# Optimization experiments

Hardware: AMD Instinct MI355X
Metric: run time of the kernel (lower is better)

## Reference

```python
import jax, jax.numpy as jnp
import numpy as np
from jax import lax

N_NODES = 100000
L_IN = 60           # raw per-node signal length
DEG = 16            # in-degree per node
HID = 256           # hidden_dim = 64 * (L_IN/15)
HEADS = 2
OUT = HID // 2      # GATConv out_feats per head
EPS_BN = 1e-5
COS_S = 4.6


def setup_inputs() -> dict:
    key = jax.random.key(0)
    k = jax.random.split(key, 12)
    E = N_NODES * DEG
    x = jax.random.normal(k[0], (N_NODES, L_IN), jnp.float32)
    src = jax.random.randint(k[1], (E,), 0, N_NODES, jnp.int32)
    # every node receives DEG incoming edges (DGL GATConv requires nonzero in-degree)
    dst = jnp.repeat(jnp.arange(N_NODES, dtype=jnp.int32), DEG)
    n = lambda i, s, sc=0.05: jax.random.normal(k[i], s, jnp.float32) * sc
    return dict(
        x=x, src=src, dst=dst,
        w1=n(2, (32, 1, 5), 0.2), b1=jnp.zeros(32, jnp.float32),
        bn1_g=jnp.ones(32, jnp.float32), bn1_b=jnp.zeros(32, jnp.float32),
        w2=n(3, (64, 32, 3), 0.1), b2=jnp.zeros(64, jnp.float32),
        bn2_g=jnp.ones(64, jnp.float32), bn2_b=jnp.zeros(64, jnp.float32),
        fc1_w=n(4, (HEADS * OUT, HID)), attn1_l=n(5, (HEADS, OUT)), attn1_r=n(6, (HEADS, OUT)),
        bias1=jnp.zeros(HEADS * OUT, jnp.float32),
        fc2_w=n(7, (HEADS * OUT, HID)), attn2_l=n(8, (HEADS, OUT)), attn2_r=n(9, (HEADS, OUT)),
        bias2=jnp.zeros(HEADS * OUT, jnp.float32),
        dbn_g=jnp.ones(3 * HID, jnp.float32), dbn_b=jnp.zeros(3 * HID, jnp.float32),
        cos_W=n(10, (HID, 3 * HID), 1.0),
    )


def _conv_bn_relu(h, w, b, g, bt, stride):
    # h: [N, Cin, T] -> [N, Cout, T'] ; BatchNorm1d uses batch statistics (train-mode forward)
    y = lax.conv_general_dilated(h, w, (stride,), 'VALID',
                                 dimension_numbers=('NCH', 'OIH', 'NCH'))
    y = y + b[None, :, None]
    m = jnp.mean(y, (0, 2), keepdims=True)
    v = jnp.var(y, (0, 2), keepdims=True)
    y = (y - m) / jnp.sqrt(v + EPS_BN) * g[None, :, None] + bt[None, :, None]
    return jax.nn.relu(y)


def _gat(h, fc_w, al, ar, bias, src, dst):
    # DGL GATConv: fc -> edge attention (leaky_relu 0.2) -> edge softmax over dst -> weighted sum + bias
    feat = (h @ fc_w.T).reshape(N_NODES, HEADS, OUT)          # [N,H,D]
    el = jnp.sum(feat * al[None], -1)                          # [N,H]
    er = jnp.sum(feat * ar[None], -1)                          # [N,H]
    e = jax.nn.leaky_relu(el[src] + er[dst], 0.2)              # [E,H]
    emax = jax.ops.segment_max(e, dst, num_segments=N_NODES)  # [N,H]
    emax = jnp.where(jnp.isfinite(emax), emax, 0.0)
    ex = jnp.exp(e - emax[dst])
    den = jax.ops.segment_sum(ex, dst, num_segments=N_NODES)  # [N,H]
    alpha = ex / jnp.maximum(den[dst], 1e-12)                  # [E,H]
    out = jax.ops.segment_sum(feat[src] * alpha[..., None], dst, num_segments=N_NODES)
    return out + bias.reshape(1, HEADS, OUT)                   # [N,H,D]


def _l2n(a):
    # F.normalize: divide by L2 norm clamped to eps
    return a / jnp.maximum(jnp.linalg.norm(a, axis=1, keepdims=True), 1e-12)


def reference(x, src, dst, w1, b1, bn1_g, bn1_b, w2, b2, bn2_g, bn2_b,
              fc1_w, attn1_l, attn1_r, bias1, fc2_w, attn2_l, attn2_r, bias2,
              dbn_g, dbn_b, cos_W):
    h = x[:, None, :]                                    # [N,1,L]
    h = _conv_bn_relu(h, w1, b1, bn1_g, bn1_b, 5)        # [N,32,12]
    h = _conv_bn_relu(h, w2, b2, bn2_g, bn2_b, 3)        # [N,64,4]
    h = h.reshape(N_NODES, HID)                          # [N,256]
    g1 = _gat(h, fc1_w, attn1_l, attn1_r, bias1, src, dst)
    h1 = (jax.nn.relu(g1) + jnp.tanh(g1) + jax.nn.log_sigmoid(g1)).reshape(N_NODES, HID)
    h2 = jnp.tanh(_gat(h1, fc2_w, attn2_l, attn2_r, bias2, src, dst)).reshape(N_NODES, HID)
    h3 = jax.nn.relu(_gat(h2, fc2_w, attn2_l, attn2_r, bias2, src, dst)).reshape(N_NODES, HID)
    hc = jnp.concatenate([h1, h2, h3], axis=1)           # [N,768]
    m = jnp.mean(hc, 0)
    v = jnp.var(hc, 0)
    hc = (hc - m) / jnp.sqrt(v + EPS_BN) * dbn_g + dbn_b
    return _l2n(hc) @ _l2n(cos_W).T * COS_S              # [N,256]
```

## Files before the change

### kernel.cpp

```cpp
#include <hip/hip_runtime.h>

#define NN 100000
#define MPAD 100096
#define NT_M 782

typedef unsigned short u16;
typedef _Float16 f16x8 __attribute__((ext_vector_type(8)));
typedef __attribute__((ext_vector_type(4))) float f32x4;

__device__ __forceinline__ u16 f2h(float f){
  union { _Float16 h; u16 u; } v; v.h=(_Float16)f; return v.u;
}
__device__ __forceinline__ float h2f(u16 u){
  union { u16 u; _Float16 h; } v; v.u=u; return (float)v.h;
}
__device__ __forceinline__ void gload16(const void* g, void* l){
  __builtin_amdgcn_global_load_lds((const __attribute__((address_space(1))) void*)g,
                                   (__attribute__((address_space(3))) void*)l, 16, 0, 0);
}
__device__ __forceinline__ void lds_fence(){
  asm volatile("s_waitcnt lgkmcnt(0)" ::: "memory");
  __builtin_amdgcn_wave_barrier();
}

template<int EPI>
__global__ __launch_bounds__(256) void k_gemm(
  const u16* __restrict__ a0, const u16* __restrict__ a1, const u16* __restrict__ a2,
  const u16* __restrict__ bmat, u16* __restrict__ cout,
  float* __restrict__ outf, const float* __restrict__ tvec,
  const float* __restrict__ rnorm, int Bstride, int KT)
{
  __shared__ u16 lds[2][2][8192];
  const int tid=threadIdx.x, lane=tid&63, wid=tid>>6;
  const int wr=wid>>1, wc=wid&1;
  const long m0=(long)blockIdx.x*128;
  const int n0=blockIdx.y*128;
  f32x4 acc[4][4]={};

  auto stageT=[&](u16* L, const u16* G, long rs){
    #pragma unroll
    for(int i=0;i<4;i++){
      int idx=i*256+tid;
      int row=idx>>3, slot=idx&7;
      int gc=(slot^(row&7))*8;
      gload16(G+(long)row*rs+gc, L+idx*8);
    }
  };
  auto stage=[&](int buf,int kt){
    const u16* Ab=(kt<4)?a0:((kt<8)?a1:a2);
    int kc=(kt&3)*64;
    stageT(lds[buf][0], Ab+m0*256+kc, 256);
    stageT(lds[buf][1], bmat+(long)n0*Bstride+kt*64, Bstride);
  };
  stage(0,0);
  __syncthreads();
  int buf=0;
  for(int kt=0;kt<KT;kt++){
    if(kt+1<KT) stage(buf^1,kt+1);
    const u16* LA=lds[buf][0]; const u16* LB=lds[buf][1];
    #pragma unroll
    for(int kk=0;kk<2;kk++){
      f16x8 av[4], bv[4];
      #pragma unroll
      for(int mf=0;mf<4;mf++){
        int r=wr*64+mf*16+(lane&15);
        av[mf]=*(const f16x8*)&LA[r*64 + (((kk*4+(lane>>4))^(r&7))*8)];
      }
      #pragma unroll
      for(int nf=0;nf<4;nf++){
        int r=wc*64+nf*16+(lane&15);
        bv[nf]=*(const f16x8*)&LB[r*64 + (((kk*4+(lane>>4))^(r&7))*8)];
      }
      #pragma unroll
      for(int mf=0;mf<4;mf++){
        #pragma unroll
        for(int nf=0;nf<4;nf++)
          acc[mf][nf]=__builtin_amdgcn_mfma_f32_16x16x32_f16(av[mf],bv[nf],acc[mf][nf],0,0,0);
      }
    }
    __syncthreads();
    buf^=1;
  }
  #pragma unroll
  for(int mf=0;mf<4;mf++){
    #pragma unroll
    for(int j=0;j<4;j++){
      long row=m0+wr*64+mf*16+((lane>>4)*4)+j;
      if(row<NN){
        #pragma unroll
        for(int nf=0;nf<4;nf++){
          int col=n0+wc*64+nf*16+(lane&15);
          float v=acc[mf][nf][j];
          if(EPI==1) outf[row*256+col]=(v+tvec[col])*rnorm[row];
          else       cout[row*256+col]=f2h(v);
        }
      }
    }
  }
}

__global__ __launch_bounds__(256) void k_xmom(const float* __restrict__ x, float* __restrict__ stats){
  int t=blockIdx.x*blockDim.x+threadIdx.x, stride=gridDim.x*blockDim.x;
  int lane=threadIdx.x&63;
  float m[5]={0,0,0,0,0};
  float c[15]={0,0,0,0,0,0,0,0,0,0,0,0,0,0,0};
  for(int n=t;n<NN;n+=stride){
    float xr[60];
    #pragma unroll
    for(int i=0;i<15;i++){
      float4 v=*(const float4*)&x[(long)n*60+i*4];
      xr[i*4]=v.x; xr[i*4+1]=v.y; xr[i*4+2]=v.z; xr[i*4+3]=v.w;
    }
    #pragma unroll
    for(int p=0;p<12;p++){
      float vv[5]={xr[5*p],xr[5*p+1],xr[5*p+2],xr[5*p+3],xr[5*p+4]};
      #pragma unroll
      for(int k=0;k<5;k++) m[k]+=vv[k];
      int idx=0;
      #pragma unroll
      for(int k=0;k<5;k++){
        #pragma unroll
        for(int k2=k;k2<5;k2++){ c[idx]+=vv[k]*vv[k2]; idx++; }
      }
    }
  }
  float vals[20];
  #pragma unroll
  for(int i=0;i<5;i++) vals[i]=m[i];
  #pragma unroll
  for(int i=0;i<15;i++) vals[5+i]=c[i];
  #pragma unroll
  for(int i=0;i<20;i++){
    float v=vals[i];
    #pragma unroll
    for(int off=32;off;off>>=1) v+=__shfl_xor(v,off);
    if(lane==0) atomicAdd(&stats[i],v);
  }
}

__global__ void k_fin1(const float* __restrict__ stats, const float* __restrict__ w1,
                       const float* __restrict__ b1, const float* __restrict__ g,
                       const float* __restrict__ bt, float* __restrict__ a1c1){
  int c=threadIdx.x;
  if(c>=32) return;
  const float inv=1.0f/(NN*12.0f);
  float mu[5];
  for(int k=0;k<5;k++) mu[k]=stats[k]*inv;
  float C[5][5];
  int idx=5;
  for(int k=0;k<5;k++) for(int k2=k;k2<5;k2++){ float v=stats[idx++]*inv; C[k][k2]=v; C[k2][k]=v; }
  float wv[5];
  for(int k=0;k<5;k++) wv[k]=w1[c*5+k];
  float bb=b1[c];
  float mean=bb, e2=bb*bb;
  for(int k=0;k<5;k++){ mean+=wv[k]*mu[k]; e2+=2.f*bb*wv[k]*mu[k]; }
  for(int k=0;k<5;k++) for(int k2=0;k2<5;k2++) e2+=wv[k]*wv[k2]*C[k][k2];
  float var=e2-mean*mean;
  float a=g[c]*rsqrtf(var+1e-5f);
  a1c1[c]=a; a1c1[32+c]=bt[c]-mean*a;
}

__global__ void k_prep(const float* __restrict__ fc1, const float* __restrict__ fc2,
                       const float* __restrict__ a1l, const float* __restrict__ a1r,
                       const float* __restrict__ a2l, const float* __restrict__ a2r,
                       float* __restrict__ vprep){
  int k=threadIdx.x;
  float acc[8]={0,0,0,0,0,0,0,0};
  for(int r=0;r<256;r++){
    int h=r>>7, c=r&127;
    float f1=fc1[r*256+k], f2=fc2[r*256+k];
    acc[0+h]+=f1*a1l[h*128+c];
    acc[2+h]+=f1*a1r[h*128+c];
    acc[4+h]+=f2*a2l[h*128+c];
    acc[6+h]+=f2*a2r[h*128+c];
  }
  #pragma unroll
  for(int v=0;v<8;v++) vprep[v*256+k]=acc[v];
}

__global__ __launch_bounds__(256) void k_conv(const float* __restrict__ x,
  const float* __restrict__ w1, const float* __restrict__ b1,
  const float* __restrict__ a1c1, const float* __restrict__ w2,
  const float* __restrict__ b2, float* __restrict__ y2, float* __restrict__ stats2)
{
  __shared__ float w2s[64*97];
  __shared__ float w1s[160], a1s[32], c1s[32], b1s[32], b2s[64];
  __shared__ float xs[4][64];
  __shared__ float z1s[4][384];
  __shared__ float bsum[128];
  int tid=threadIdx.x, lane=tid&63, w=tid>>6;
  for(int i=tid;i<6144;i+=256) w2s[(i/96)*97+(i%96)]=w2[i];
  if(tid<160) w1s[tid]=w1[tid];
  if(tid<32){ a1s[tid]=a1c1[tid]; c1s[tid]=a1c1[32+tid]; b1s[tid]=b1[tid]; }
  if(tid<64) b2s[tid]=b2[tid];
  if(tid<128) bsum[tid]=0.f;
  __syncthreads();
  float ssum=0.f, ssq=0.f;
  int gw=blockIdx.x*4+w, nw=gridDim.x*4;
  for(int n=gw;n<NN;n+=nw){
    if(lane<60) xs[w][lane]=x[(long)n*60+lane];
    lds_fence();
    {
      int c=lane>>1, pb=(lane&1)*6;
      float av=a1s[c], cv=c1s[c], bb=b1s[c];
      #pragma unroll
      for(int i=0;i<6;i++){
        int p=pb+i;
        float y=bb;
        #pragma unroll
        for(int k=0;k<5;k++) y+=xs[w][5*p+k]*w1s[c*5+k];
        z1s[w][c*12+p]=fmaxf(y*av+cv,0.f);
      }
    }
    lds_fence();
    {
      int c2=lane;
      float acc0=b2s[c2],acc1=b2s[c2],acc2=b2s[c2],acc3=b2s[c2];
      #pragma unroll
      for(int ci=0;ci<32;ci++){
        float4 za=*(const float4*)&z1s[w][ci*12];
        float4 zb=*(const float4*)&z1s[w][ci*12+4];
        float4 zc=*(const float4*)&z1s[w][ci*12+8];
        float w0=w2s[c2*97+ci*3], wv1=w2s[c2*97+ci*3+1], wv2=w2s[c2*97+ci*3+2];
        acc0 += za.x*w0+za.y*wv1+za.z*wv2;
        acc1 += za.w*w0+zb.x*wv1+zb.y*wv2;
        acc2 += zb.z*w0+zb.w*wv1+zc.x*wv2;
        acc3 += zc.y*w0+zc.z*wv1+zc.w*wv2;
      }
      float4 o; o.x=acc0; o.y=acc1; o.z=acc2; o.w=acc3;
      *(float4*)&y2[(long)n*256+c2*4]=o;
      ssum+=acc0+acc1+acc2+acc3;
      ssq+=acc0*acc0+acc1*acc1+acc2*acc2+acc3*acc3;
    }
    lds_fence();
  }
  atomicAdd(&bsum[lane],ssum);
  atomicAdd(&bsum[64+lane],ssq);
  __syncthreads();
  if(tid<128) atomicAdd(&stats2[tid],bsum[tid]);
}

__global__ void k_fin2(const float* __restrict__ stats2, const float* __restrict__ g,
                       const float* __restrict__ bt, float* __restrict__ a2c2){
  int c=threadIdx.x;
  if(c>=64) return;
  const float inv=1.0f/(NN*4.0f);
  float mean=stats2[c]*inv;
  float var=stats2[64+c]*inv-mean*mean;
  float a=g[c]*rsqrtf(var+1e-5f);
  a2c2[c]=a; a2c2[64+c]=bt[c]-mean*a;
}

__global__ __launch_bounds__(256) void k_happ(const float* __restrict__ y2,
  const float* __restrict__ a2c2, const float* __restrict__ vprep,
  u16* __restrict__ h, float* __restrict__ elv, float* __restrict__ erv)
{
  int lane=threadIdx.x&63;
  int gw=blockIdx.x*4+(threadIdx.x>>6), nw=gridDim.x*4;
  float a2=a2c2[lane], c2v=a2c2[64+lane];
  int cb=lane*4;
  float4 vl0=*(const float4*)&vprep[cb];
  float4 vl1=*(const float4*)&vprep[256+cb];
  float4 vr0=*(const float4*)&vprep[512+cb];
  float4 vr1=*(const float4*)&vprep[768+cb];
  for(int n=gw;n<NN;n+=nw){
    float4 y=*(const float4*)&y2[(long)n*256+cb];
    float o0=fmaxf(y.x*a2+c2v,0.f), o1=fmaxf(y.y*a2+c2v,0.f);
    float o2=fmaxf(y.z*a2+c2v,0.f), o3=fmaxf(y.w*a2+c2v,0.f);
    ushort4 o; o.x=f2h(o0); o.y=f2h(o1); o.z=f2h(o2); o.w=f2h(o3);
    *(ushort4*)&h[(long)n*256+cb]=o;
    float pl0=o0*vl0.x+o1*vl0.y+o2*vl0.z+o3*vl0.w;
    float pl1=o0*vl1.x+o1*vl1.y+o2*vl1.z+o3*vl1.w;
    float pr0=o0*vr0.x+o1*vr0.y+o2*vr0.z+o3*vr0.w;
    float pr1=o0*vr1.x+o1*vr1.y+o2*vr1.z+o3*vr1.w;
    #pragma unroll
    for(int off=32;off;off>>=1){
      pl0+=__shfl_xor(pl0,off); pl1+=__shfl_xor(pl1,off);
      pr0+=__shfl_xor(pr0,off); pr1+=__shfl_xor(pr1,off);
    }
    if(lane==0){ elv[2*n]=pl0; elv[2*n+1]=pl1; erv[2*n]=pr0; erv[2*n+1]=pr1; }
  }
}

__global__ void k_cvth(const float* __restrict__ in, u16* __restrict__ out, int n){
  int i=blockIdx.x*blockDim.x+threadIdx.x;
  if(i<n) out[i]=f2h(in[i]);
}

__global__ __launch_bounds__(256) void k_wfold(const float* __restrict__ cw, const float* __restrict__ ab,
  u16* __restrict__ wh, float* __restrict__ tvec)
{
  int lane=threadIdx.x&63;
  int r=blockIdx.x*4+(threadIdx.x>>6);
  if(r>=256) return;
  float v[12]; float ss=0.f, tn=0.f;
  #pragma unroll
  for(int i=0;i<12;i++){
    int col=i*64+lane;
    v[i]=cw[r*768+col];
    ss+=v[i]*v[i];
    tn+=v[i]*ab[768+col];
  }
  #pragma unroll
  for(int off=32;off;off>>=1){ ss+=__shfl_xor(ss,off); tn+=__shfl_xor(tn,off); }
  float sc=1.0f/fmaxf(sqrtf(ss),1e-12f);
  #pragma unroll
  for(int i=0;i<12;i++){
    int col=i*64+lane;
    wh[r*768+col]=f2h(v[i]*sc*ab[col]);
  }
  if(lane==0) tvec[r]=tn*sc;
}

__global__ __launch_bounds__(256) void k_alpha(const float* __restrict__ el, const float* __restrict__ er,
  const int* __restrict__ srcv, float* __restrict__ alpha)
{
  int n=blockIdx.x*blockDim.x+threadIdx.x;
  if(n>=NN) return;
  int sidx[16];
  #pragma unroll
  for(int j=0;j<16;j+=4){
    int4 v=*(const int4*)&srcv[n*16+j];
    sidx[j]=v.x; sidx[j+1]=v.y; sidx[j+2]=v.z; sidx[j+3]=v.w;
  }
  float er0=er[2*n], er1=er[2*n+1];
  float e0[16], e1[16];
  float mx0=-1e30f, mx1=-1e30f;
  #pragma unroll
  for(int j=0;j<16;j++){
    float a=el[2*sidx[j]]+er0;
    float bb=el[2*sidx[j]+1]+er1;
    a = a>0.f? a : 0.2f*a;
    bb = bb>0.f? bb : 0.2f*bb;
    e0[j]=a; e1[j]=bb;
    mx0=fmaxf(mx0,a); mx1=fmaxf(mx1,bb);
  }
  float d0=0.f,d1=0.f;
  #pragma unroll
  for(int j=0;j<16;j++){
    e0[j]=__expf(e0[j]-mx0); d0+=e0[j];
    e1[j]=__expf(e1[j]-mx1); d1+=e1[j];
  }
  float r0=1.f/fmaxf(d0,1e-12f), r1=1.f/fmaxf(d1,1e-12f);
  #pragma unroll
  for(int j=0;j<16;j++){
    float2 o; o.x=e0[j]*r0; o.y=e1[j]*r1;
    ((float2*)alpha)[(long)n*16+j]=o;
  }
}

template<int ACT> __device__ __forceinline__ float actf(float g);
template<> __device__ __forceinline__ float actf<1>(float g){
  float t=tanhf(g);
  float ls=fminf(g,0.f)-log1pf(__expf(-fabsf(g)));
  return fmaxf(g,0.f)+t+ls;
}
template<> __device__ __forceinline__ float actf<2>(float g){ return tanhf(g); }
template<> __device__ __forceinline__ float actf<3>(float g){ return fmaxf(g,0.f); }

template<int ACT,int WELR>
__global__ __launch_bounds__(256) void k_aggr(const u16* __restrict__ fH,
  const float* __restrict__ alpha, const int* __restrict__ srcv, const float* __restrict__ bias,
  u16* __restrict__ hH, float* __restrict__ dbn_raw, int col_base,
  const float* __restrict__ vnext, float* __restrict__ elo, float* __restrict__ ero)
{
  __shared__ float bsum[256], bsq[256];
  int tid=threadIdx.x, lane=tid&63;
  bsum[tid]=0.f; bsq[tid]=0.f;
  __syncthreads();
  int gw=blockIdx.x*4+(tid>>6), nw=gridDim.x*4;
  int head=lane>>5, cb=lane*4;
  float4 b4=*(const float4*)&bias[cb];
  float4 vl0={0,0,0,0},vl1={0,0,0,0},vr0={0,0,0,0},vr1={0,0,0,0};
  if(WELR){
    vl0=*(const float4*)&vnext[cb];
    vl1=*(const float4*)&vnext[256+cb];
    vr0=*(const float4*)&vnext[512+cb];
    vr1=*(const float4*)&vnext[768+cb];
  }
  float s[4]={0,0,0,0}, q[4]={0,0,0,0};
  for(int n=gw;n<NN;n+=nw){
    int sidx[16];
    #pragma unroll
    for(int j=0;j<16;j+=4){
      int4 v=*(const int4*)&srcv[n*16+j];
      sidx[j]=v.x; sidx[j+1]=v.y; sidx[j+2]=v.z; sidx[j+3]=v.w;
    }
    float a0=b4.x,a1=b4.y,a2=b4.z,a3=b4.w;
    #pragma unroll
    for(int j=0;j<16;j++){
      float2 aw2=((const float2*)alpha)[(long)n*16+j];
      float aw = head? aw2.y : aw2.x;
      ushort4 f=*(const ushort4*)&fH[(long)sidx[j]*256+cb];
      a0+=aw*h2f(f.x); a1+=aw*h2f(f.y);
      a2+=aw*h2f(f.z); a3+=aw*h2f(f.w);
    }
    float h0=actf<ACT>(a0), h1=actf<ACT>(a1), h2=actf<ACT>(a2), h3=actf<ACT>(a3);
    ushort4 o; o.x=f2h(h0); o.y=f2h(h1); o.z=f2h(h2); o.w=f2h(h3);
    *(ushort4*)&hH[(long)n*256+cb]=o;
    s[0]+=h0; s[1]+=h1; s[2]+=h2; s[3]+=h3;
    q[0]+=h0*h0; q[1]+=h1*h1; q[2]+=h2*h2; q[3]+=h3*h3;
    if(WELR){
      float pl0=h0*vl0.x+h1*vl0.y+h2*vl0.z+h3*vl0.w;
      float pl1=h0*vl1.x+h1*vl1.y+h2*vl1.z+h3*vl1.w;
      float pr0=h0*vr0.x+h1*vr0.y+h2*vr0.z+h3*vr0.w;
      float pr1=h0*vr1.x+h1*vr1.y+h2*vr1.z+h3*vr1.w;
      #pragma unroll
      for(int off2=32;off2;off2>>=1){
        pl0+=__shfl_xor(pl0,off2); pl1+=__shfl_xor(pl1,off2);
        pr0+=__shfl_xor(pr0,off2); pr1+=__shfl_xor(pr1,off2);
      }
      if(lane==0){ elo[2*n]=pl0; elo[2*n+1]=pl1; ero[2*n]=pr0; ero[2*n+1]=pr1; }
    }
  }
  #pragma unroll
  for(int i=0;i<4;i++){ atomicAdd(&bsum[cb+i], s[i]); atomicAdd(&bsq[cb+i], q[i]); }
  __syncthreads();
  atomicAdd(&dbn_raw[col_base+tid], bsum[tid]);
  atomicAdd(&dbn_raw[768+col_base+tid], bsq[tid]);
}

__global__ void k_dbnfin(const float* __restrict__ raw, const float* __restrict__ g,
                         const float* __restrict__ b, float* __restrict__ ab){
  int c=blockIdx.x*blockDim.x+threadIdx.x;
  if(c<768){
    float mean=raw[c]*(1.0f/NN);
    float var=raw[768+c]*(1.0f/NN)-mean*mean;
    float a=g[c]*rsqrtf(var+1e-5f);
    ab[c]=a; ab[768+c]=b[c]-mean*a;
  }
}

__global__ __launch_bounds__(256) void k_rnorm(
  const u16* __restrict__ h1h, const u16* __restrict__ h2h, const u16* __restrict__ h3h,
  const float* __restrict__ ab, float* __restrict__ rn)
{
  int lane=threadIdx.x&63;
  int gw=blockIdx.x*4+(threadIdx.x>>6), nw=gridDim.x*4;
  int cb=lane*4;
  float av[12], cv[12];
  #pragma unroll
  for(int s=0;s<3;s++){
    #pragma unroll
    for(int i=0;i<4;i++){ av[s*4+i]=ab[s*256+cb+i]; cv[s*4+i]=ab[768+s*256+cb+i]; }
  }
  for(int n=gw;n<NN;n+=nw){
    float ss=0.f;
    const u16* hh[3]={h1h,h2h,h3h};
    #pragma unroll
    for(int s=0;s<3;s++){
      ushort4 a4=*(const ushort4*)&hh[s][(long)n*256+cb];
      float o0=h2f(a4.x)*av[s*4+0]+cv[s*4+0];
      float o1=h2f(a4.y)*av[s*4+1]+cv[s*4+1];
      float o2=h2f(a4.z)*av[s*4+2]+cv[s*4+2];
      float o3=h2f(a4.w)*av[s*4+3]+cv[s*4+3];
      ss+=o0*o0+o1*o1+o2*o2+o3*o3;
    }
    #pragma unroll
    for(int off=32;off;off>>=1) ss+=__shfl_xor(ss,off);
    if(lane==0) rn[n]=4.6f/fmaxf(sqrtf(ss),1e-12f);
  }
}

extern "C" void kernel_launch(void* const* d_in, const int* in_sizes, int n_in,
                              void* d_out, int out_size, void* d_ws, size_t ws_size,
                              hipStream_t stream)
{
  (void)in_sizes; (void)n_in; (void)out_size; (void)ws_size;
  const float* x   =(const float*)d_in[0];
  const int*   src =(const int*)d_in[1];
  const float* w1  =(const float*)d_in[3];
  const float* b1  =(const float*)d_in[4];
  const float* bn1g=(const float*)d_in[5];
  const float* bn1b=(const float*)d_in[6];
  const float* w2  =(const float*)d_in[7];
  const float* b2  =(const float*)d_in[8];
  const float* bn2g=(const float*)d_in[9];
  const float* bn2b=(const float*)d_in[10];
  const float* fc1 =(const float*)d_in[11];
  const float* a1l =(const float*)d_in[12];
  const float* a1r =(const float*)d_in[13];
  const float* bias1=(const float*)d_in[14];
  const float* fc2 =(const float*)d_in[15];
  const float* a2l =(const float*)d_in[16];
  const float* a2r =(const float*)d_in[17];
  const float* bias2=(const float*)d_in[18];
  const float* dbng=(const float*)d_in[19];
  const float* dbnb=(const float*)d_in[20];
  const float* cw  =(const float*)d_in[21];

  char* ws=(char*)d_ws;
  size_t off=0;
  auto take=[&](size_t bytes)->char*{ char* p=ws+off; off=(off+bytes+255)&~(size_t)255; return p; };
  float* stats =(float*)take(2048*4);
  float* params=(float*)take(4096*4);
  float* el    =(float*)take((size_t)MPAD*2*4);
  float* er    =(float*)take((size_t)MPAD*2*4);
  float* rnorm =(float*)take((size_t)MPAD*4);
  float* tvec  =(float*)take(256*4);
  float* alpha =(float*)take((size_t)NN*32*4);
  u16* fc1h=(u16*)take((size_t)65536*2);
  u16* fc2h=(u16*)take((size_t)65536*2);
  u16* wfh =(u16*)take((size_t)196608*2);
  float* y2 =(float*)take((size_t)MPAD*256*4);
  const size_t FB=(size_t)MPAD*256*2;
  u16* h0H  =(u16*)take(FB);
  u16* h1H  =(u16*)take(FB);
  u16* h2H  =(u16*)take(FB);
  u16* featH=(u16*)d_out;

  float* xmom   =stats;
  float* stats2 =stats+32;
  float* dbn_raw=stats+512;
  float* a1c1   =params;
  float* a2c2   =params+64;
  float* dbn_ab =params+256;
  float* vprep  =params+2048;

  hipMemsetAsync(stats,0,2048*4,stream);
  k_cvth<<<dim3(256),dim3(256),0,stream>>>(fc1,fc1h,65536);
  k_cvth<<<dim3(256),dim3(256),0,stream>>>(fc2,fc2h,65536);
  k_prep<<<dim3(1),dim3(256),0,stream>>>(fc1,fc2,a1l,a1r,a2l,a2r,vprep);
  k_xmom<<<dim3(128),dim3(256),0,stream>>>(x,xmom);
  k_fin1<<<dim3(1),dim3(64),0,stream>>>(xmom,w1,b1,bn1g,bn1b,a1c1);
  k_conv<<<dim3(1024),dim3(256),0,stream>>>(x,w1,b1,a1c1,w2,b2,y2,stats2);
  k_fin2<<<dim3(1),dim3(64),0,stream>>>(stats2,bn2g,bn2b,a2c2);
  k_happ<<<dim3(2048),dim3(256),0,stream>>>(y2,a2c2,vprep,h0H,el,er);

  dim3 gg(NT_M,2);
  k_gemm<0><<<gg,dim3(256),0,stream>>>(h0H,h0H,h0H,fc1h,featH,(float*)nullptr,tvec,rnorm,256,4);
  k_alpha<<<dim3(391),dim3(256),0,stream>>>(el,er,src,alpha);
  k_aggr<1,1><<<dim3(2048),dim3(256),0,stream>>>(featH,alpha,src,bias1,h1H,dbn_raw,0,
                                                 vprep+1024,el,er);
  k_gemm<0><<<gg,dim3(256),0,stream>>>(h1H,h1H,h1H,fc2h,featH,(float*)nullptr,tvec,rnorm,256,4);
  k_alpha<<<dim3(391),dim3(256),0,stream>>>(el,er,src,alpha);
  k_aggr<2,1><<<dim3(2048),dim3(256),0,stream>>>(featH,alpha,src,bias2,h2H,dbn_raw,256,
                                                 vprep+1024,el,er);
  k_gemm<0><<<gg,dim3(256),0,stream>>>(h2H,h2H,h2H,fc2h,featH,(float*)nullptr,tvec,rnorm,256,4);
  k_alpha<<<dim3(391),dim3(256),0,stream>>>(el,er,src,alpha);
  k_aggr<3,0><<<dim3(2048),dim3(256),0,stream>>>(featH,alpha,src,bias2,h0H,dbn_raw,512,
                                                 vprep+1024,el,er);
  k_dbnfin<<<dim3(3),dim3(256),0,stream>>>(dbn_raw,dbng,dbnb,dbn_ab);
  k_wfold<<<dim3(64),dim3(256),0,stream>>>(cw,dbn_ab,wfh,tvec);
  k_rnorm<<<dim3(1024),dim3(256),0,stream>>>(h1H,h2H,h0H,dbn_ab,rnorm);
  k_gemm<1><<<gg,dim3(256),0,stream>>>(h1H,h2H,h0H,wfh,(u16*)nullptr,
                                       (float*)d_out,tvec,rnorm,768,12);
}
```

Measured before the change: 1.259 ms.

## Recast second conv layer as fp16 MFMA GEMM with fused column statistics

```diff
diff --git a/kernel.cpp b/kernel.cpp
--- a/kernel.cpp
+++ b/kernel.cpp
@@ -28,14 +28,17 @@
   const u16* __restrict__ a0, const u16* __restrict__ a1, const u16* __restrict__ a2,
   const u16* __restrict__ bmat, u16* __restrict__ cout,
   float* __restrict__ outf, const float* __restrict__ tvec,
-  const float* __restrict__ rnorm, int Bstride, int KT)
+  const float* __restrict__ rnorm, float* __restrict__ colstats,
+  int CW, int Bstride, int KT)
 {
   __shared__ u16 lds[2][2][8192];
+  __shared__ float cstat[256];
   const int tid=threadIdx.x, lane=tid&63, wid=tid>>6;
   const int wr=wid>>1, wc=wid&1;
   const long m0=(long)blockIdx.x*128;
   const int n0=blockIdx.y*128;
   f32x4 acc[4][4]={};
+  if(EPI==2) cstat[tid]=0.f;
 
   auto stageT=[&](u16* L, const u16* G, long rs){
     #pragma unroll
@@ -47,10 +50,12 @@
     }
   };
   auto stage=[&](int buf,int kt){
-    const u16* Ab=(kt<4)?a0:((kt<8)?a1:a2);
-    int kc=(kt&3)*64;
-    stageT(lds[buf][0], Ab+m0*256+kc, 256);
-    stageT(lds[buf][1], bmat+(long)n0*Bstride+kt*64, Bstride);
+    int kg=kt*64;
+    int chn=kg/CW;
+    int kc=kg-chn*CW;
+    const u16* Ab = (chn==0)?a0:((chn==1)?a1:a2);
+    stageT(lds[buf][0], Ab+m0*CW+kc, CW);
+    stageT(lds[buf][1], bmat+(long)n0*Bstride+kg, Bstride);
   };
   stage(0,0);
   __syncthreads();
@@ -81,6 +86,7 @@
     __syncthreads();
     buf^=1;
   }
+  float csum[4]={0,0,0,0}, csq[4]={0,0,0,0};
   #pragma unroll
   for(int mf=0;mf<4;mf++){
     #pragma unroll
@@ -92,9 +98,23 @@
           int col=n0+wc*64+nf*16+(lane&15);
           float v=acc[mf][nf][j];
           if(EPI==1) outf[row*256+col]=(v+tvec[col])*rnorm[row];
-          else       cout[row*256+col]=f2h(v);
+          else if(EPI==2){ outf[row*256+col]=v; csum[nf]+=v; csq[nf]+=v*v; }
+          else cout[row*256+col]=f2h(v);
         }
       }
+    }
+  }
+  if(EPI==2){
+    #pragma unroll
+    for(int nf=0;nf<4;nf++){
+      int lc=wc*64+nf*16+(lane&15);
+      atomicAdd(&cstat[lc],csum[nf]);
+      atomicAdd(&cstat[128+lc],csq[nf]);
+    }
+    __syncthreads();
+    if(tid<128){
+      atomicAdd(&colstats[n0+tid],cstat[tid]);
+      atomicAdd(&colstats[256+n0+tid],cstat[128+tid]);
     }
   }
 }
@@ -178,75 +198,62 @@
   for(int v=0;v<8;v++) vprep[v*256+k]=acc[v];
 }
 
-__global__ __launch_bounds__(256) void k_conv(const float* __restrict__ x,
+__global__ void k_w2d(const float* __restrict__ w2, u16* __restrict__ wd){
+  int j=threadIdx.x;
+  if(j>=256) return;
+  int c2=j>>2, p=j&3;
+  for(int t=0;t<384;t++) wd[j*384+t]=0;
+  for(int ci=0;ci<32;ci++)
+    for(int k=0;k<3;k++)
+      wd[j*384 + ci*12 + 3*p + k]=f2h(w2[(c2*32+ci)*3+k]);
+}
+
+__global__ __launch_bounds__(256) void k_z1(const float* __restrict__ x,
   const float* __restrict__ w1, const float* __restrict__ b1,
-  const float* __restrict__ a1c1, const float* __restrict__ w2,
-  const float* __restrict__ b2, float* __restrict__ y2, float* __restrict__ stats2)
-{
-  __shared__ float w2s[64*97];
-  __shared__ float w1s[160], a1s[32], c1s[32], b1s[32], b2s[64];
+  const float* __restrict__ a1c1, u16* __restrict__ z1)
+{
+  __shared__ float w1s[160], a1s[32], c1s[32], b1s[32];
   __shared__ float xs[4][64];
-  __shared__ float z1s[4][384];
-  __shared__ float bsum[128];
   int tid=threadIdx.x, lane=tid&63, w=tid>>6;
-  for(int i=tid;i<6144;i+=256) w2s[(i/96)*97+(i%96)]=w2[i];
   if(tid<160) w1s[tid]=w1[tid];
   if(tid<32){ a1s[tid]=a1c1[tid]; c1s[tid]=a1c1[32+tid]; b1s[tid]=b1[tid]; }
-  if(tid<64) b2s[tid]=b2[tid];
-  if(tid<128) bsum[tid]=0.f;
   __syncthreads();
-  float ssum=0.f, ssq=0.f;
   int gw=blockIdx.x*4+w, nw=gridDim.x*4;
+  int c=lane>>1, pb=(lane&1)*6;
+  float av=a1s[c], cv=c1s[c], bb=b1s[c];
+  float wv[5];
+  #pragma unroll
+  for(int k=0;k<5;k++) wv[k]=w1s[c*5+k];
   for(int n=gw;n<NN;n+=nw){
     if(lane<60) xs[w][lane]=x[(long)n*60+lane];
     lds_fence();
-    {
-      int c=lane>>1, pb=(lane&1)*6;
-      float av=a1s[c], cv=c1s[c], bb=b1s[c];
-      #pragma unroll
-      for(int i=0;i<6;i++){
-        int p=pb+i;
-        float y=bb;
-        #pragma unroll
-        for(int k=0;k<5;k++) y+=xs[w][5*p+k]*w1s[c*5+k];
-        z1s[w][c*12+p]=fmaxf(y*av+cv,0.f);
-      }
-    }
+    ushort2 zz[3];
+    #pragma unroll
+    for(int i=0;i<6;i++){
+      int p=pb+i;
+      float y=bb;
+      #pragma unroll
+      for(int k=0;k<5;k++) y+=xs[w][5*p+k]*wv[k];
+      u16 h=f2h(fmaxf(y*av+cv,0.f));
+      if(i&1) zz[i>>1].y=h; else zz[i>>1].x=h;
+    }
+    long base=(long)n*384 + c*12 + pb;
+    *(ushort2*)&z1[base]  =zz[0];
+    *(ushort2*)&z1[base+2]=zz[1];
+    *(ushort2*)&z1[base+4]=zz[2];
     lds_fence();
-    {
-      int c2=lane;
-      float acc0=b2s[c2],acc1=b2s[c2],acc2=b2s[c2],acc3=b2s[c2];
-      #pragma unroll
-      for(int ci=0;ci<32;ci++){
-        float4 za=*(const float4*)&z1s[w][ci*12];
-        float4 zb=*(const float4*)&z1s[w][ci*12+4];
-        float4 zc=*(const float4*)&z1s[w][ci*12+8];
-        float w0=w2s[c2*97+ci*3], wv1=w2s[c2*97+ci*3+1], wv2=w2s[c2*97+ci*3+2];
-        acc0 += za.x*w0+za.y*wv1+za.z*wv2;
-        acc1 += za.w*w0+zb.x*wv1+zb.y*wv2;
-        acc2 += zb.z*w0+zb.w*wv1+zc.x*wv2;
-        acc3 += zc.y*w0+zc.z*wv1+zc.w*wv2;
-      }
-      float4 o; o.x=acc0; o.y=acc1; o.z=acc2; o.w=acc3;
-      *(float4*)&y2[(long)n*256+c2*4]=o;
-      ssum+=acc0+acc1+acc2+acc3;
-      ssq+=acc0*acc0+acc1*acc1+acc2*acc2+acc3*acc3;
-    }
-    lds_fence();
-  }
-  atomicAdd(&bsum[lane],ssum);
-  atomicAdd(&bsum[64+lane],ssq);
-  __syncthreads();
-  if(tid<128) atomicAdd(&stats2[tid],bsum[tid]);
-}
-
-__global__ void k_fin2(const float* __restrict__ stats2, const float* __restrict__ g,
+  }
+}
+
+__global__ void k_fin2(const float* __restrict__ cs, const float* __restrict__ g,
                        const float* __restrict__ bt, float* __restrict__ a2c2){
   int c=threadIdx.x;
   if(c>=64) return;
+  float s=cs[4*c]+cs[4*c+1]+cs[4*c+2]+cs[4*c+3];
+  float q=cs[256+4*c]+cs[256+4*c+1]+cs[256+4*c+2]+cs[256+4*c+3];
   const float inv=1.0f/(NN*4.0f);
-  float mean=stats2[c]*inv;
-  float var=stats2[64+c]*inv-mean*mean;
+  float mean=s*inv;
+  float var=q*inv-mean*mean;
   float a=g[c]*rsqrtf(var+1e-5f);
   a2c2[c]=a; a2c2[64+c]=bt[c]-mean*a;
 }
@@ -492,7 +499,7 @@
   char* ws=(char*)d_ws;
   size_t off=0;
   auto take=[&](size_t bytes)->char*{ char* p=ws+off; off=(off+bytes+255)&~(size_t)255; return p; };
-  float* stats =(float*)take(2048*4);
+  float* stats =(float*)take(4096*4);
   float* params=(float*)take(4096*4);
   float* el    =(float*)take((size_t)MPAD*2*4);
   float* er    =(float*)take((size_t)MPAD*2*4);
@@ -502,6 +509,8 @@
   u16* fc1h=(u16*)take((size_t)65536*2);
   u16* fc2h=(u16*)take((size_t)65536*2);
   u16* wfh =(u16*)take((size_t)196608*2);
+  u16* w2d =(u16*)take((size_t)98304*2);
+  u16* z1  =(u16*)take((size_t)MPAD*384*2);
   float* y2 =(float*)take((size_t)MPAD*256*4);
   const size_t FB=(size_t)MPAD*256*2;
   u16* h0H  =(u16*)take(FB);
@@ -510,33 +519,40 @@
   u16* featH=(u16*)d_out;
 
   float* xmom   =stats;
-  float* stats2 =stats+32;
-  float* dbn_raw=stats+512;
+  float* stats2 =stats+64;
+  float* dbn_raw=stats+1024;
   float* a1c1   =params;
   float* a2c2   =params+64;
   float* dbn_ab =params+256;
   float* vprep  =params+2048;
 
-  hipMemsetAsync(stats,0,2048*4,stream);
+  hipMemsetAsync(stats,0,4096*4,stream);
   k_cvth<<<dim3(256),dim3(256),0,stream>>>(fc1,fc1h,65536);
   k_cvth<<<dim3(256),dim3(256),0,stream>>>(fc2,fc2h,65536);
   k_prep<<<dim3(1),dim3(256),0,stream>>>(fc1,fc2,a1l,a1r,a2l,a2r,vprep);
+  k_w2d<<<dim3(1),dim3(256),0,stream>>>(w2,w2d);
   k_xmom<<<dim3(128),dim3(256),0,stream>>>(x,xmom);
   k_fin1<<<dim3(1),dim3(64),0,stream>>>(xmom,w1,b1,bn1g,bn1b,a1c1);
-  k_conv<<<dim3(1024),dim3(256),0,stream>>>(x,w1,b1,a1c1,w2,b2,y2,stats2);
+  k_z1<<<dim3(1024),dim3(256),0,stream>>>(x,w1,b1,a1c1,z1);
+
+  dim3 gg(NT_M,2);
+  k_gemm<2><<<gg,dim3(256),0,stream>>>(z1,z1,z1,w2d,(u16*)nullptr,y2,
+                                       (float*)nullptr,(float*)nullptr,stats2,384,384,6);
   k_fin2<<<dim3(1),dim3(64),0,stream>>>(stats2,bn2g,bn2b,a2c2);
   k_happ<<<dim3(2048),dim3(256),0,stream>>>(y2,a2c2,vprep,h0H,el,er);
 
-  dim3 gg(NT_M,2);
-  k_gemm<0><<<gg,dim3(256),0,stream>>>(h0H,h0H,h0H,fc1h,featH,(float*)nullptr,tvec,rnorm,256,4);
+  k_gemm<0><<<gg,dim3(256),0,stream>>>(h0H,h0H,h0H,fc1h,featH,(float*)nullptr,
+                                       (float*)nullptr,(float*)nullptr,(float*)nullptr,256,256,4);
   k_alpha<<<dim3(391),dim3(256),0,stream>>>(el,er,src,alpha);
   k_aggr<1,1><<<dim3(2048),dim3(256),0,stream>>>(featH,alpha,src,bias1,h1H,dbn_raw,0,
                                                  vprep+1024,el,er);
-  k_gemm<0><<<gg,dim3(256),0,stream>>>(h1H,h1H,h1H,fc2h,featH,(float*)nullptr,tvec,rnorm,256,4);
+  k_gemm<0><<<gg,dim3(256),0,stream>>>(h1H,h1H,h1H,fc2h,featH,(float*)nullptr,
+                                       (float*)nullptr,(float*)nullptr,(float*)nullptr,256,256,4);
   k_alpha<<<dim3(391),dim3(256),0,stream>>>(el,er,src,alpha);
   k_aggr<2,1><<<dim3(2048),dim3(256),0,stream>>>(featH,alpha,src,bias2,h2H,dbn_raw,256,
                                                  vprep+1024,el,er);
-  k_gemm<0><<<gg,dim3(256),0,stream>>>(h2H,h2H,h2H,fc2h,featH,(float*)nullptr,tvec,rnorm,256,4);
+  k_gemm<0><<<gg,dim3(256),0,stream>>>(h2H,h2H,h2H,fc2h,featH,(float*)nullptr,
+                                       (float*)nullptr,(float*)nullptr,(float*)nullptr,256,256,4);
   k_alpha<<<dim3(391),dim3(256),0,stream>>>(el,er,src,alpha);
   k_aggr<3,0><<<dim3(2048),dim3(256),0,stream>>>(featH,alpha,src,bias2,h0H,dbn_raw,512,
                                                  vprep+1024,el,er);
@@ -544,5 +560,5 @@
   k_wfold<<<dim3(64),dim3(256),0,stream>>>(cw,dbn_ab,wfh,tvec);
   k_rnorm<<<dim3(1024),dim3(256),0,stream>>>(h1H,h2H,h0H,dbn_ab,rnorm);
   k_gemm<1><<<gg,dim3(256),0,stream>>>(h1H,h2H,h0H,wfh,(u16*)nullptr,
-                                       (float*)d_out,tvec,rnorm,768,12);
-}
+                                       (float*)d_out,tvec,rnorm,(float*)nullptr,256,768,12);
+}
```

Result: slower. 1.497 ms (+18.9%).
